# Kernel tuning notes

Measured on AMD Instinct MI355X. Metric: run time of the kernel, lower is better.

## Reference

```python
import jax, jax.numpy as jnp
import numpy as np

N_NODES = 50000
N_EDGES = 800000
N_SCALES = 4
D_IN = 128
D_HID = 128


def gcn_conv(x, W, b, src, dst, ew, n):
    # PyG GCNConv: h = x @ W; add self loops (weight 1); symmetric normalization
    # deg computed over destination with edge weights; out = scatter(norm * h[src]) + b
    h = x @ W
    loops = jnp.arange(n)
    src_f = jnp.concatenate([src, loops])
    dst_f = jnp.concatenate([dst, loops])
    ew_f = jnp.concatenate([ew, jnp.ones((n,), x.dtype)])
    deg = jax.ops.segment_sum(ew_f, dst_f, num_segments=n)
    dinv = jnp.where(deg > 0, jax.lax.rsqrt(deg), jnp.zeros((), x.dtype))
    norm = dinv[src_f] * ew_f * dinv[dst_f]  # [E+n]
    out = jax.ops.segment_sum(h[src_f] * norm[:, None], dst_f, num_segments=n)
    return out + b


def setup_inputs() -> dict:
    key = jax.random.key(0)
    ks = jax.random.split(key, 8)
    x = jax.random.normal(ks[0], (N_NODES, D_IN), dtype=jnp.float32)
    edge_index = jax.random.randint(ks[1], (N_SCALES, 2, N_EDGES), 0, N_NODES, dtype=jnp.int64)
    edge_weight = jax.random.uniform(ks[2], (N_SCALES, N_EDGES), dtype=jnp.float32)
    s = 1.0 / np.sqrt(D_IN)
    W0 = jax.random.uniform(ks[3], (D_IN, D_HID), jnp.float32, -s, s)
    b0 = jnp.zeros((D_HID,), jnp.float32)
    W1 = jax.random.uniform(ks[4], (D_HID, D_HID), jnp.float32, -s, s)
    b1 = jnp.zeros((D_HID,), jnp.float32)
    prelu_a = 0.25 * jnp.ones((D_HID,), jnp.float32)  # torch PReLU default init
    return {"x": x, "edge_index": edge_index, "edge_weight": edge_weight,
            "W0": W0, "b0": b0, "W1": W1, "b1": b1, "prelu_a": prelu_a}


def reference(x, edge_index, edge_weight, W0, b0, W1, b1, prelu_a):
    n = x.shape[0]
    prelu = lambda z: jnp.where(z > 0, z, prelu_a * z)
    outs = []
    for t in range(edge_index.shape[0]):  # small fixed number of scales
        src, dst = edge_index[t, 0], edge_index[t, 1]
        ew = edge_weight[t]
        z = prelu(gcn_conv(x, W0, b0, src, dst, ew, n))
        z = prelu(gcn_conv(z, W1, b1, src, dst, ew, n))
        outs.append(z)
    return jnp.stack(outs)  # [nm_scale, N, hidden]
```

## Files before the change

kernel.cpp:

```cpp
#include <hip/hip_runtime.h>

#define NN 50000
#define NE 800000
#define NS 4
#define NT (NS * NN)
#define D 128
#define SB2 782
#define EW_SCALE 262144.0f
#define EW_INV (1.0f / 262144.0f)

typedef unsigned long long ull;
typedef __attribute__((ext_vector_type(8))) short bf16x8;
typedef __attribute__((ext_vector_type(4))) float f32x4;

__device__ __forceinline__ unsigned short f2bf(float f) {
  unsigned int u = __float_as_uint(f);
  u += 0x7fffu + ((u >> 16) & 1u);
  return (unsigned short)(u >> 16);
}
__device__ __forceinline__ float bf2f(unsigned short h) {
  return __uint_as_float((unsigned int)h << 16);
}

__global__ __launch_bounds__(256) void fused_cpg_k(
    const int* __restrict__ ei, const float* __restrict__ ewA,
    ull* __restrict__ pack8, int* __restrict__ posA,
    const float* __restrict__ X, const float* __restrict__ W0,
    unsigned short* __restrict__ H0h,
    const float* __restrict__ W1, unsigned short* __restrict__ Wsw) {
  __shared__ float xs[64 * 130];
  __shared__ float ws[32 * 128];
  const int bx = blockIdx.x;
  const int t = blockIdx.y;
  const int tid = threadIdx.x;

  if (bx < 782) {
    const int e0 = bx * 1024 + tid;
    const size_t cOff = (size_t)(bx & 7) * NT;
    const int* dst = ei + (size_t)t * 2 * NE + NE;
    const float* ew = ewA + (size_t)t * NE;
    int d[4];
    float w[4];
    bool va[4];
#pragma unroll
    for (int q = 0; q < 4; q++) {
      int e = e0 + q * 256;
      va[q] = e < NE;
      d[q] = 0;
      w[q] = 0.f;
      if (va[q]) {
        d[q] = dst[e];
        w[q] = ew[e];
      }
    }
    ull old[4];
#pragma unroll
    for (int q = 0; q < 4; q++) {
      if (va[q]) {
        ull add = (1ULL << 32) | (ull)__float2uint_rn(w[q] * EW_SCALE);
        old[q] = atomicAdd(&pack8[cOff + t * NN + d[q]], add);
      }
    }
#pragma unroll
    for (int q = 0; q < 4; q++) {
      if (va[q]) posA[(size_t)t * NE + e0 + q * 256] = (int)(old[q] >> 32);
    }
    return;
  }
  if (t != 0) return;

  if (bx < 1564) {
    const int r0 = (bx - 782) * 64;
    for (int i = tid; i < 64 * 64; i += 256) {
      int row = i >> 6, kh = i & 63;
      float2 v = make_float2(0.f, 0.f);
      int gr = r0 + row;
      if (gr < NN) v = *(const float2*)&X[(size_t)gr * D + kh * 2];
      *(float2*)&xs[row * 130 + kh * 2] = v;
    }
    const int tx = tid & 15, ty = tid >> 4;
    const int c0 = tx * 4;
    const int c1 = 64 + tx * 4;
    float acc[4][8];
#pragma unroll
    for (int i = 0; i < 4; i++)
#pragma unroll
      for (int j = 0; j < 8; j++) acc[i][j] = 0.f;

    for (int kc = 0; kc < 4; kc++) {
      __syncthreads();
      for (int i = tid; i < 32 * 32; i += 256) {
        ((float4*)ws)[i] = ((const float4*)(W0 + kc * 32 * D))[i];
      }
      __syncthreads();
#pragma unroll 4
      for (int k2 = 0; k2 < 32; k2++) {
        const int k = kc * 32 + k2;
        float a[4];
#pragma unroll
        for (int j = 0; j < 4; j++) a[j] = xs[(ty * 4 + j) * 130 + k];
        float4 b0 = *(const float4*)&ws[k2 * 128 + c0];
        float4 b1 = *(const float4*)&ws[k2 * 128 + c1];
        float b[8] = {b0.x, b0.y, b0.z, b0.w, b1.x, b1.y, b1.z, b1.w};
#pragma unroll
        for (int i = 0; i < 4; i++)
#pragma unroll
          for (int j = 0; j < 8; j++) acc[i][j] += a[i] * b[j];
      }
    }
#pragma unroll
    for (int i = 0; i < 4; i++) {
      int gr = r0 + ty * 4 + i;
      if (gr < NN) {
        ushort4 o0, o1;
        o0.x = f2bf(acc[i][0]); o0.y = f2bf(acc[i][1]);
        o0.z = f2bf(acc[i][2]); o0.w = f2bf(acc[i][3]);
        o1.x = f2bf(acc[i][4]); o1.y = f2bf(acc[i][5]);
        o1.z = f2bf(acc[i][6]); o1.w = f2bf(acc[i][7]);
        *(ushort4*)&H0h[(size_t)gr * D + c0] = o0;
        *(ushort4*)&H0h[(size_t)gr * D + c1] = o1;
      }
    }
  } else {
    int idx = (bx - 1564) * 256 + tid;
    int j = idx & 7, lane = (idx >> 3) & 63, s = (idx >> 9) & 3, bn = idx >> 11;
    float v = W1[(s * 32 + ((lane >> 4) * 8) + j) * D + bn * 16 + (lane & 15)];
    unsigned short hi = f2bf(v);
    float lo = v - bf2f(hi);
    Wsw[idx] = hi;
    Wsw[16384 + idx] = f2bf(lo);
  }
}

__global__ __launch_bounds__(256) void gemm_inplace_mfma_k(
    unsigned short* __restrict__ ZhA, const unsigned short* __restrict__ Wsw) {
  const int t = blockIdx.y;
  unsigned short* Z = ZhA + (size_t)t * NN * D;
  const int tid = threadIdx.x;
  const int wv = tid >> 6, l = tid & 63;
  const int r0 = blockIdx.x * 64 + wv * 16;
  const int mrow = r0 + (l & 15);
  const int arow = mrow < NN ? mrow : NN - 1;
  bf16x8 a[4];
#pragma unroll
  for (int s = 0; s < 4; s++)
    a[s] = *(const bf16x8*)&Z[(size_t)arow * D + s * 32 + (l >> 4) * 8];
  const int orow0 = r0 + (l >> 4) * 4;
#pragma unroll
  for (int bn = 0; bn < 8; bn++) {
    f32x4 acc = {0.f, 0.f, 0.f, 0.f};
#pragma unroll
    for (int s = 0; s < 4; s++) {
      bf16x8 blo = *(const bf16x8*)&Wsw[16384 + ((bn * 4 + s) * 64 + l) * 8];
      bf16x8 bhi = *(const bf16x8*)&Wsw[((bn * 4 + s) * 64 + l) * 8];
      acc = __builtin_amdgcn_mfma_f32_16x16x32_bf16(a[s], blo, acc, 0, 0, 0);
      acc = __builtin_amdgcn_mfma_f32_16x16x32_bf16(a[s], bhi, acc, 0, 0, 0);
    }
    const int col = bn * 16 + (l & 15);
#pragma unroll
    for (int i = 0; i < 4; i++) {
      int row = orow0 + i;
      if (row < NN) Z[(size_t)row * D + col] = f2bf(acc[i]);
    }
  }
}


__global__ __launch_bounds__(256) void initp_k(ull* __restrict__ packed, int n) {
  int i = blockIdx.x * 256 + threadIdx.x;
  if (i < n) packed[i] = 0ULL;
}

__global__ __launch_bounds__(256) void unpack_scan_k(const ull* __restrict__ pack8,
                                                     float* __restrict__ dinvA,
                                                     int* __restrict__ cntA,
                                                     unsigned short* __restrict__ cbase8,
                                                     int* __restrict__ partial) {
  __shared__ int sm[256];
  const int tid = threadIdx.x;
  const int i = blockIdx.x * 256 + tid;
  int c = 0;
  if (i < NT) {
    unsigned int wsum = 0;
    int run = 0;
#pragma unroll
    for (int k = 0; k < 8; k++) {
      ull p = pack8[(size_t)k * NT + i];
      cbase8[(size_t)k * NT + i] = (unsigned short)run;
      run += (int)(p >> 32);
      wsum += (unsigned int)(p & 0xffffffffULL);
    }
    c = run;
    cntA[i] = c;
    float deg = 1.0f + (float)wsum * EW_INV;
    dinvA[i] = rsqrtf(deg);
  }
  sm[tid] = c;
  __syncthreads();
  for (int off = 128; off > 0; off >>= 1) {
    if (tid < off) sm[tid] += sm[tid + off];
    __syncthreads();
  }
  if (tid == 0) partial[blockIdx.x] = sm[0];
}

__global__ __launch_bounds__(256) void scan_write_k(const int* __restrict__ cntA,
                                                    const int* __restrict__ partial,
                                                    int* __restrict__ offsA) {
  __shared__ int sm[256];
  const int t = threadIdx.x;
  const int bx = blockIdx.x;
  int s = 0;
  for (int i = t; i < bx; i += 256) s += partial[i];
  sm[t] = s;
  __syncthreads();
  for (int off = 128; off > 0; off >>= 1) {
    if (t < off) sm[t] += sm[t + off];
    __syncthreads();
  }
  const int base = sm[0];
  __syncthreads();
  const int i = bx * 256 + t;
  int v = (i < NT) ? cntA[i] : 0;
  sm[t] = v;
  __syncthreads();
  for (int off = 1; off < 256; off <<= 1) {
    int u = (t >= off) ? sm[t - off] : 0;
    __syncthreads();
    sm[t] += u;
    __syncthreads();
  }
  if (i < NT) offsA[i] = base + sm[t] - v;
}

__global__ __launch_bounds__(256) void fill_all_k(const int* __restrict__ ei,
                                                  const float* __restrict__ ewA,
                                                  const float* __restrict__ dinvA,
                                                  const int* __restrict__ offsA,
                                                  const int* __restrict__ posA,
                                                  const unsigned short* __restrict__ cbase8,
                                                  int2* __restrict__ eeA) {
  const int t = blockIdx.y;
  const int e = blockIdx.x * 256 + threadIdx.x;
  if (e < NE) {
    const int* src = ei + (size_t)t * 2 * NE;
    const int* dst = src + NE;
    int s = src[e], d = dst[e];
    const int base = t * NN + d;
    const size_t cOff = (size_t)((e >> 10) & 7) * NT;
    float w = ewA[(size_t)t * NE + e] * dinvA[t * NN + s] * dinvA[base];
    int slot = offsA[base] + (int)cbase8[cOff + base] + posA[(size_t)t * NE + e];
    eeA[slot] = make_int2(s, __float_as_int(w));
  }
}

__global__ __launch_bounds__(256) void gather1_all_k(
    const unsigned short* __restrict__ H, const int* __restrict__ offsA,
    const int* __restrict__ cntA, const int2* __restrict__ eeA,
    const float* __restrict__ dinvA, const float* __restrict__ bias,
    const float* __restrict__ pa, unsigned short* __restrict__ ZhA) {
  const int t = blockIdx.y;
  int g = blockIdx.x * 256 + threadIdx.x;
  int wid = g >> 5;
  int lane = g & 31;
  if (wid >= NN) return;
  const int base = t * NN + wid;
  const int st = offsA[base];
  const int len = cntA[base];
  const int c = lane * 4;
  float ax = 0.f, ay = 0.f, az = 0.f, aw = 0.f;
  int j = 0;
  for (; j + 8 <= len; j += 8) {
    int2 p0 = eeA[st + j];
    int2 p1 = eeA[st + j + 1];
    int2 p2 = eeA[st + j + 2];
    int2 p3 = eeA[st + j + 3];
    int2 p4 = eeA[st + j + 4];
    int2 p5 = eeA[st + j + 5];
    int2 p6 = eeA[st + j + 6];
    int2 p7 = eeA[st + j + 7];
    ushort4 v0 = *(const ushort4*)&H[(size_t)p0.x * D + c];
    ushort4 v1 = *(const ushort4*)&H[(size_t)p1.x * D + c];
    ushort4 v2 = *(const ushort4*)&H[(size_t)p2.x * D + c];
    ushort4 v3 = *(const ushort4*)&H[(size_t)p3.x * D + c];
    ushort4 v4 = *(const ushort4*)&H[(size_t)p4.x * D + c];
    ushort4 v5 = *(const ushort4*)&H[(size_t)p5.x * D + c];
    ushort4 v6 = *(const ushort4*)&H[(size_t)p6.x * D + c];
    ushort4 v7 = *(const ushort4*)&H[(size_t)p7.x * D + c];
    float w0 = __int_as_float(p0.y), w1 = __int_as_float(p1.y);
    float w2 = __int_as_float(p2.y), w3 = __int_as_float(p3.y);
    float w4 = __int_as_float(p4.y), w5 = __int_as_float(p5.y);
    float w6 = __int_as_float(p6.y), w7 = __int_as_float(p7.y);
    ax += w0 * bf2f(v0.x) + w1 * bf2f(v1.x) + w2 * bf2f(v2.x) + w3 * bf2f(v3.x);
    ay += w0 * bf2f(v0.y) + w1 * bf2f(v1.y) + w2 * bf2f(v2.y) + w3 * bf2f(v3.y);
    az += w0 * bf2f(v0.z) + w1 * bf2f(v1.z) + w2 * bf2f(v2.z) + w3 * bf2f(v3.z);
    aw += w0 * bf2f(v0.w) + w1 * bf2f(v1.w) + w2 * bf2f(v2.w) + w3 * bf2f(v3.w);
    ax += w4 * bf2f(v4.x) + w5 * bf2f(v5.x) + w6 * bf2f(v6.x) + w7 * bf2f(v7.x);
    ay += w4 * bf2f(v4.y) + w5 * bf2f(v5.y) + w6 * bf2f(v6.y) + w7 * bf2f(v7.y);
    az += w4 * bf2f(v4.z) + w5 * bf2f(v5.z) + w6 * bf2f(v6.z) + w7 * bf2f(v7.z);
    aw += w4 * bf2f(v4.w) + w5 * bf2f(v5.w) + w6 * bf2f(v6.w) + w7 * bf2f(v7.w);
  }
  for (; j + 4 <= len; j += 4) {
    int2 p0 = eeA[st + j];
    int2 p1 = eeA[st + j + 1];
    int2 p2 = eeA[st + j + 2];
    int2 p3 = eeA[st + j + 3];
    ushort4 v0 = *(const ushort4*)&H[(size_t)p0.x * D + c];
    ushort4 v1 = *(const ushort4*)&H[(size_t)p1.x * D + c];
    ushort4 v2 = *(const ushort4*)&H[(size_t)p2.x * D + c];
    ushort4 v3 = *(const ushort4*)&H[(size_t)p3.x * D + c];
    float w0 = __int_as_float(p0.y), w1 = __int_as_float(p1.y);
    float w2 = __int_as_float(p2.y), w3 = __int_as_float(p3.y);
    ax += w0 * bf2f(v0.x) + w1 * bf2f(v1.x) + w2 * bf2f(v2.x) + w3 * bf2f(v3.x);
    ay += w0 * bf2f(v0.y) + w1 * bf2f(v1.y) + w2 * bf2f(v2.y) + w3 * bf2f(v3.y);
    az += w0 * bf2f(v0.z) + w1 * bf2f(v1.z) + w2 * bf2f(v2.z) + w3 * bf2f(v3.z);
    aw += w0 * bf2f(v0.w) + w1 * bf2f(v1.w) + w2 * bf2f(v2.w) + w3 * bf2f(v3.w);
  }
  for (; j < len; j++) {
    int2 p = eeA[st + j];
    float w = __int_as_float(p.y);
    ushort4 v = *(const ushort4*)&H[(size_t)p.x * D + c];
    ax += w * bf2f(v.x);
    ay += w * bf2f(v.y);
    az += w * bf2f(v.z);
    aw += w * bf2f(v.w);
  }
  float dv = dinvA[base];
  float d2 = dv * dv;
  ushort4 h = *(const ushort4*)&H[(size_t)wid * D + c];
  ax += d2 * bf2f(h.x) + bias[c];
  ay += d2 * bf2f(h.y) + bias[c + 1];
  az += d2 * bf2f(h.z) + bias[c + 2];
  aw += d2 * bf2f(h.w) + bias[c + 3];
  ax = ax > 0.f ? ax : pa[c] * ax;
  ay = ay > 0.f ? ay : pa[c + 1] * ay;
  az = az > 0.f ? az : pa[c + 2] * az;
  aw = aw > 0.f ? aw : pa[c + 3] * aw;
  ushort4 o;
  o.x = f2bf(ax); o.y = f2bf(ay); o.z = f2bf(az); o.w = f2bf(aw);
  *(ushort4*)&ZhA[(size_t)t * NN * D + (size_t)wid * D + c] = o;
}

__global__ __launch_bounds__(256) void gather2_all_k(
    const unsigned short* __restrict__ YA, const int* __restrict__ offsA,
    const int* __restrict__ cntA, const int2* __restrict__ eeA,
    const float* __restrict__ dinvA, const float* __restrict__ bias,
    const float* __restrict__ pa, float* __restrict__ out) {
  const int t = blockIdx.y;
  int g = blockIdx.x * 256 + threadIdx.x;
  int wid = g >> 5;
  int lane = g & 31;
  if (wid >= NN) return;
  const unsigned short* Y = YA + (size_t)t * NN * D;
  const int base = t * NN + wid;
  const int st = offsA[base];
  const int len = cntA[base];
  const int c = lane * 4;
  float ax = 0.f, ay = 0.f, az = 0.f, aw = 0.f;
  int j = 0;
  for (; j + 8 <= len; j += 8) {
    int2 p0 = eeA[st + j];
    int2 p1 = eeA[st + j + 1];
    int2 p2 = eeA[st + j + 2];
    int2 p3 = eeA[st + j + 3];
    int2 p4 = eeA[st + j + 4];
    int2 p5 = eeA[st + j + 5];
    int2 p6 = eeA[st + j + 6];
    int2 p7 = eeA[st + j + 7];
    ushort4 v0 = *(const ushort4*)&Y[(size_t)p0.x * D + c];
    ushort4 v1 = *(const ushort4*)&Y[(size_t)p1.x * D + c];
    ushort4 v2 = *(const ushort4*)&Y[(size_t)p2.x * D + c];
    ushort4 v3 = *(const ushort4*)&Y[(size_t)p3.x * D + c];
    ushort4 v4 = *(const ushort4*)&Y[(size_t)p4.x * D + c];
    ushort4 v5 = *(const ushort4*)&Y[(size_t)p5.x * D + c];
    ushort4 v6 = *(const ushort4*)&Y[(size_t)p6.x * D + c];
    ushort4 v7 = *(const ushort4*)&Y[(size_t)p7.x * D + c];
    float w0 = __int_as_float(p0.y), w1 = __int_as_float(p1.y);
    float w2 = __int_as_float(p2.y), w3 = __int_as_float(p3.y);
    float w4 = __int_as_float(p4.y), w5 = __int_as_float(p5.y);
    float w6 = __int_as_float(p6.y), w7 = __int_as_float(p7.y);
    ax += w0 * bf2f(v0.x) + w1 * bf2f(v1.x) + w2 * bf2f(v2.x) + w3 * bf2f(v3.x);
    ay += w0 * bf2f(v0.y) + w1 * bf2f(v1.y) + w2 * bf2f(v2.y) + w3 * bf2f(v3.y);
    az += w0 * bf2f(v0.z) + w1 * bf2f(v1.z) + w2 * bf2f(v2.z) + w3 * bf2f(v3.z);
    aw += w0 * bf2f(v0.w) + w1 * bf2f(v1.w) + w2 * bf2f(v2.w) + w3 * bf2f(v3.w);
    ax += w4 * bf2f(v4.x) + w5 * bf2f(v5.x) + w6 * bf2f(v6.x) + w7 * bf2f(v7.x);
    ay += w4 * bf2f(v4.y) + w5 * bf2f(v5.y) + w6 * bf2f(v6.y) + w7 * bf2f(v7.y);
    az += w4 * bf2f(v4.z) + w5 * bf2f(v5.z) + w6 * bf2f(v6.z) + w7 * bf2f(v7.z);
    aw += w4 * bf2f(v4.w) + w5 * bf2f(v5.w) + w6 * bf2f(v6.w) + w7 * bf2f(v7.w);
  }
  for (; j + 4 <= len; j += 4) {
    int2 p0 = eeA[st + j];
    int2 p1 = eeA[st + j + 1];
    int2 p2 = eeA[st + j + 2];
    int2 p3 = eeA[st + j + 3];
    ushort4 v0 = *(const ushort4*)&Y[(size_t)p0.x * D + c];
    ushort4 v1 = *(const ushort4*)&Y[(size_t)p1.x * D + c];
    ushort4 v2 = *(const ushort4*)&Y[(size_t)p2.x * D + c];
    ushort4 v3 = *(const ushort4*)&Y[(size_t)p3.x * D + c];
    float w0 = __int_as_float(p0.y), w1 = __int_as_float(p1.y);
    float w2 = __int_as_float(p2.y), w3 = __int_as_float(p3.y);
    ax += w0 * bf2f(v0.x) + w1 * bf2f(v1.x) + w2 * bf2f(v2.x) + w3 * bf2f(v3.x);
    ay += w0 * bf2f(v0.y) + w1 * bf2f(v1.y) + w2 * bf2f(v2.y) + w3 * bf2f(v3.y);
    az += w0 * bf2f(v0.z) + w1 * bf2f(v1.z) + w2 * bf2f(v2.z) + w3 * bf2f(v3.z);
    aw += w0 * bf2f(v0.w) + w1 * bf2f(v1.w) + w2 * bf2f(v2.w) + w3 * bf2f(v3.w);
  }
  for (; j < len; j++) {
    int2 p = eeA[st + j];
    float w = __int_as_float(p.y);
    ushort4 v = *(const ushort4*)&Y[(size_t)p.x * D + c];
    ax += w * bf2f(v.x);
    ay += w * bf2f(v.y);
    az += w * bf2f(v.z);
    aw += w * bf2f(v.w);
  }
  float dv = dinvA[base];
  float d2 = dv * dv;
  ushort4 h = *(const ushort4*)&Y[(size_t)wid * D + c];
  ax += d2 * bf2f(h.x) + bias[c];
  ay += d2 * bf2f(h.y) + bias[c + 1];
  az += d2 * bf2f(h.z) + bias[c + 2];
  aw += d2 * bf2f(h.w) + bias[c + 3];
  ax = ax > 0.f ? ax : pa[c] * ax;
  ay = ay > 0.f ? ay : pa[c + 1] * ay;
  az = az > 0.f ? az : pa[c + 2] * az;
  aw = aw > 0.f ? aw : pa[c + 3] * aw;
  float* outT = out + (size_t)t * NN * D;
  *(float4*)&outT[(size_t)wid * D + c] = make_float4(ax, ay, az, aw);
}


extern "C" void kernel_launch(void* const* d_in, const int* in_sizes, int n_in,
                              void* d_out, int out_size, void* d_ws, size_t ws_size,
                              hipStream_t stream) {
  const float* x = (const float*)d_in[0];
  const int* ei = (const int*)d_in[1];
  const float* ew = (const float*)d_in[2];
  const float* W0 = (const float*)d_in[3];
  const float* b0 = (const float*)d_in[4];
  const float* W1 = (const float*)d_in[5];
  const float* b1 = (const float*)d_in[6];
  const float* pa = (const float*)d_in[7];
  float* out = (float*)d_out;

  int2* eeA = (int2*)d_ws;
  int* posA = (int*)(eeA + (size_t)NS * NE);
  float* dinvA = (float*)(posA + (size_t)NS * NE);
  int* cntA = (int*)(dinvA + NT);
  int* offsA = cntA + NT;
  int* partial = offsA + NT;
  int* poffs = partial + 1024;
  unsigned short* H0h = (unsigned short*)(poffs + 1024);
  unsigned short* ZhA = H0h + (size_t)NN * D;
  unsigned short* Wsw = ZhA + (size_t)NS * NN * D;
  unsigned short* cbase8 = ZhA;
  ull* pack8 = (ull*)(ZhA + (size_t)8 * NT);

  const int gGemm = (NN + 63) / 64;
  const int gEdge = (NE + 255) / 256;
  const int gInit8 = (8 * NT) / 256;
  const int gGather = (NN * 32 + 255) / 256;
  const int gFused = 782 + 782 + 64;

  initp_k<<<gInit8, 256, 0, stream>>>(pack8, 8 * NT);
  fused_cpg_k<<<dim3(gFused, NS), 256, 0, stream>>>(ei, ew, pack8, posA,
                                                    x, W0, H0h, W1, Wsw);

  unpack_scan_k<<<SB2, 256, 0, stream>>>(pack8, dinvA, cntA, cbase8, partial);
  scan_write_k<<<SB2, 256, 0, stream>>>(cntA, partial, offsA);
  fill_all_k<<<dim3(gEdge, NS), 256, 0, stream>>>(ei, ew, dinvA, offsA, posA,
                                                  cbase8, eeA);

  gather1_all_k<<<dim3(gGather, NS), 256, 0, stream>>>(H0h, offsA, cntA, eeA,
                                                       dinvA, b0, pa, ZhA);
  gemm_inplace_mfma_k<<<dim3(gGemm, NS), 256, 0, stream>>>(ZhA, Wsw);
  gather2_all_k<<<dim3(gGather, NS), 256, 0, stream>>>(ZhA, offsA, cntA, eeA,
                                                       dinvA, b1, pa, out);
}
```

Before: 700.3 us.

## Build CSR via two-level binned counting sort with LDS histograms instead of global atomics

Replaces the global 64-bit atomic counting pass, the multi-kernel scan and the posA-based fill with a radix-style binning sort. Edges are first histogrammed by dst>>8 into shared-memory bins per block and the per-bin histograms are scanned. Edges are then scattered into bins, and each bin is sorted locally in LDS to produce the CSR, degrees and dinv, followed by a normalization pass. This aims to cut contended global atomics and random global writes, at the cost of more kernel launches, an extra edge-array pass, and packing dst and src into 16 bits each (dst<<16|s). That packing only works because node ids fit in 16 bits (NN=50000) and LDS atomics keep the edge order non-deterministic.

```diff
diff --git a/kernel.cpp b/kernel.cpp
--- a/kernel.cpp
+++ b/kernel.cpp
@@ -5,10 +5,12 @@
 #define NS 4
 #define NT (NS * NN)
 #define D 128
-#define SB2 782
+#define NB 196
+#define CB 782
 #define EW_SCALE 262144.0f
 #define EW_INV (1.0f / 262144.0f)
 
+typedef unsigned int u32;
 typedef unsigned long long ull;
 typedef __attribute__((ext_vector_type(8))) short bf16x8;
 typedef __attribute__((ext_vector_type(4))) float f32x4;
@@ -22,55 +24,35 @@
   return __uint_as_float((unsigned int)h << 16);
 }
 
-__global__ __launch_bounds__(256) void fused_cpg_k(
-    const int* __restrict__ ei, const float* __restrict__ ewA,
-    ull* __restrict__ pack8, int* __restrict__ posA,
+__global__ __launch_bounds__(256) void fused_hg_k(
+    const int* __restrict__ ei, u32* __restrict__ ghist,
     const float* __restrict__ X, const float* __restrict__ W0,
     unsigned short* __restrict__ H0h,
     const float* __restrict__ W1, unsigned short* __restrict__ Wsw) {
   __shared__ float xs[64 * 130];
   __shared__ float ws[32 * 128];
+  __shared__ u32 h[NB];
   const int bx = blockIdx.x;
   const int t = blockIdx.y;
   const int tid = threadIdx.x;
 
-  if (bx < 782) {
-    const int e0 = bx * 1024 + tid;
-    const size_t cOff = (size_t)(bx & 7) * NT;
+  if (bx < CB) {
+    if (tid < NB) h[tid] = 0;
+    __syncthreads();
     const int* dst = ei + (size_t)t * 2 * NE + NE;
-    const float* ew = ewA + (size_t)t * NE;
-    int d[4];
-    float w[4];
-    bool va[4];
 #pragma unroll
     for (int q = 0; q < 4; q++) {
-      int e = e0 + q * 256;
-      va[q] = e < NE;
-      d[q] = 0;
-      w[q] = 0.f;
-      if (va[q]) {
-        d[q] = dst[e];
-        w[q] = ew[e];
-      }
-    }
-    ull old[4];
-#pragma unroll
-    for (int q = 0; q < 4; q++) {
-      if (va[q]) {
-        ull add = (1ULL << 32) | (ull)__float2uint_rn(w[q] * EW_SCALE);
-        old[q] = atomicAdd(&pack8[cOff + t * NN + d[q]], add);
-      }
-    }
-#pragma unroll
-    for (int q = 0; q < 4; q++) {
-      if (va[q]) posA[(size_t)t * NE + e0 + q * 256] = (int)(old[q] >> 32);
-    }
+      int e = bx * 1024 + q * 256 + tid;
+      if (e < NE) atomicAdd(&h[(u32)dst[e] >> 8], 1u);
+    }
+    __syncthreads();
+    if (tid < NB) ghist[((size_t)t * NB + tid) * CB + bx] = h[tid];
     return;
   }
   if (t != 0) return;
 
-  if (bx < 1564) {
-    const int r0 = (bx - 782) * 64;
+  if (bx < 2 * CB) {
+    const int r0 = (bx - CB) * 64;
     for (int i = tid; i < 64 * 64; i += 256) {
       int row = i >> 6, kh = i & 63;
       float2 v = make_float2(0.f, 0.f);
@@ -122,13 +104,155 @@
       }
     }
   } else {
-    int idx = (bx - 1564) * 256 + tid;
+    int idx = (bx - 2 * CB) * 256 + tid;
     int j = idx & 7, lane = (idx >> 3) & 63, s = (idx >> 9) & 3, bn = idx >> 11;
     float v = W1[(s * 32 + ((lane >> 4) * 8) + j) * D + bn * 16 + (lane & 15)];
     unsigned short hi = f2bf(v);
     float lo = v - bf2f(hi);
     Wsw[idx] = hi;
     Wsw[16384 + idx] = f2bf(lo);
+  }
+}
+
+__global__ __launch_bounds__(256) void scanbin_k(u32* __restrict__ ghist,
+                                                 u32* __restrict__ bincnt) {
+  __shared__ int sm[256];
+  const int b = blockIdx.x, t = blockIdx.y, tid = threadIdx.x;
+  u32* g = ghist + ((size_t)t * NB + b) * CB;
+  const int lo = tid * 4;
+  const int hi = min(lo + 4, CB);
+  int s = 0;
+  for (int i = lo; i < hi; i++) s += (int)g[i];
+  sm[tid] = s;
+  __syncthreads();
+  for (int off = 1; off < 256; off <<= 1) {
+    int u = (tid >= off) ? sm[tid - off] : 0;
+    __syncthreads();
+    sm[tid] += u;
+    __syncthreads();
+  }
+  int run = sm[tid] - s;
+  for (int i = lo; i < hi; i++) {
+    u32 v = g[i];
+    g[i] = (u32)run;
+    run += (int)v;
+  }
+  if (lo < CB && hi == CB) bincnt[t * NB + b] = (u32)run;
+}
+
+__global__ __launch_bounds__(256) void binbase_k(const u32* __restrict__ bincnt,
+                                                 u32* __restrict__ binbase) {
+  __shared__ int sm[256];
+  const int t = blockIdx.y, tid = threadIdx.x;
+  int v = (tid < NB) ? (int)bincnt[t * NB + tid] : 0;
+  sm[tid] = v;
+  __syncthreads();
+  for (int off = 1; off < 256; off <<= 1) {
+    int u = (tid >= off) ? sm[tid - off] : 0;
+    __syncthreads();
+    sm[tid] += u;
+    __syncthreads();
+  }
+  if (tid < NB) binbase[t * NB + tid] = (u32)(sm[tid] - v);
+}
+
+__global__ __launch_bounds__(256) void scat_k(const int* __restrict__ ei,
+                                              const float* __restrict__ ewA,
+                                              const u32* __restrict__ ghist,
+                                              const u32* __restrict__ binbase,
+                                              int2* __restrict__ ebin) {
+  __shared__ u32 c[NB];
+  __shared__ int bb[NB];
+  const int bx = blockIdx.x, t = blockIdx.y, tid = threadIdx.x;
+  if (tid < NB) {
+    c[tid] = ghist[((size_t)t * NB + tid) * CB + bx];
+    bb[tid] = (int)binbase[t * NB + tid];
+  }
+  __syncthreads();
+  const int* src = ei + (size_t)t * 2 * NE;
+  const int* dst = src + NE;
+  const float* ew = ewA + (size_t)t * NE;
+  int2* eb = ebin + (size_t)t * NE;
+#pragma unroll
+  for (int q = 0; q < 4; q++) {
+    int e = bx * 1024 + q * 256 + tid;
+    if (e < NE) {
+      u32 d = (u32)dst[e];
+      u32 s = (u32)src[e];
+      float w = ew[e];
+      u32 bin = d >> 8;
+      u32 r = atomicAdd(&c[bin], 1u);
+      eb[bb[bin] + r] = make_int2((int)((d << 16) | s), __float_as_int(w));
+    }
+  }
+}
+
+__global__ __launch_bounds__(256) void bincsr_k(const int2* __restrict__ ebin,
+                                                const u32* __restrict__ bincnt,
+                                                const u32* __restrict__ binbase,
+                                                int* __restrict__ cntA,
+                                                int* __restrict__ offsA,
+                                                float* __restrict__ dinvA,
+                                                int2* __restrict__ eeA) {
+  __shared__ u32 cnt[256];
+  __shared__ u32 wsum[256];
+  __shared__ u32 c2[256];
+  __shared__ int sm[256];
+  __shared__ int excls[256];
+  const int b = blockIdx.x, t = blockIdx.y, tid = threadIdx.x;
+  const int m = (int)bincnt[t * NB + b];
+  const int bb = (int)binbase[t * NB + b];
+  const int2* eb = ebin + (size_t)t * NE + bb;
+  cnt[tid] = 0;
+  wsum[tid] = 0;
+  c2[tid] = 0;
+  __syncthreads();
+  for (int i = tid; i < m; i += 256) {
+    int2 r = eb[i];
+    u32 dl = ((u32)r.x >> 16) & 255u;
+    atomicAdd(&cnt[dl], 1u);
+    atomicAdd(&wsum[dl], (u32)__float2uint_rn(__int_as_float(r.y) * EW_SCALE));
+  }
+  __syncthreads();
+  int v = (int)cnt[tid];
+  sm[tid] = v;
+  __syncthreads();
+  for (int off = 1; off < 256; off <<= 1) {
+    int u = (tid >= off) ? sm[tid - off] : 0;
+    __syncthreads();
+    sm[tid] += u;
+    __syncthreads();
+  }
+  const int excl = sm[tid] - v;
+  excls[tid] = excl;
+  const int g = b * 256 + tid;
+  if (g < NN) {
+    cntA[t * NN + g] = v;
+    offsA[t * NN + g] = t * NE + bb + excl;
+    float deg = 1.0f + (float)wsum[tid] * EW_INV;
+    dinvA[t * NN + g] = rsqrtf(deg);
+  }
+  __syncthreads();
+  int2* ee = eeA + (size_t)t * NE + bb;
+  for (int i = tid; i < m; i += 256) {
+    int2 r = eb[i];
+    u32 dl = ((u32)r.x >> 16) & 255u;
+    u32 rk = atomicAdd(&c2[dl], 1u);
+    ee[excls[dl] + (int)rk] = r;
+  }
+}
+
+__global__ __launch_bounds__(256) void rescale_k(const float* __restrict__ dinvA,
+                                                 int2* __restrict__ eeA) {
+  const int t = blockIdx.y;
+  const int e = blockIdx.x * 256 + threadIdx.x;
+  if (e < NE) {
+    int2 r = eeA[(size_t)t * NE + e];
+    int s = r.x & 0xffff;
+    int d = (int)((u32)r.x >> 16);
+    const float* dv = dinvA + t * NN;
+    float w = __int_as_float(r.y) * dv[s] * dv[d];
+    eeA[(size_t)t * NE + e] = make_int2(s, __float_as_int(w));
   }
 }
 
@@ -162,95 +286,6 @@
       int row = orow0 + i;
       if (row < NN) Z[(size_t)row * D + col] = f2bf(acc[i]);
     }
-  }
-}
-
-
-__global__ __launch_bounds__(256) void initp_k(ull* __restrict__ packed, int n) {
-  int i = blockIdx.x * 256 + threadIdx.x;
-  if (i < n) packed[i] = 0ULL;
-}
-
-__global__ __launch_bounds__(256) void unpack_scan_k(const ull* __restrict__ pack8,
-                                                     float* __restrict__ dinvA,
-                                                     int* __restrict__ cntA,
-                                                     unsigned short* __restrict__ cbase8,
-                                                     int* __restrict__ partial) {
-  __shared__ int sm[256];
-  const int tid = threadIdx.x;
-  const int i = blockIdx.x * 256 + tid;
-  int c = 0;
-  if (i < NT) {
-    unsigned int wsum = 0;
-    int run = 0;
-#pragma unroll
-    for (int k = 0; k < 8; k++) {
-      ull p = pack8[(size_t)k * NT + i];
-      cbase8[(size_t)k * NT + i] = (unsigned short)run;
-      run += (int)(p >> 32);
-      wsum += (unsigned int)(p & 0xffffffffULL);
-    }
-    c = run;
-    cntA[i] = c;
-    float deg = 1.0f + (float)wsum * EW_INV;
-    dinvA[i] = rsqrtf(deg);
-  }
-  sm[tid] = c;
-  __syncthreads();
-  for (int off = 128; off > 0; off >>= 1) {
-    if (tid < off) sm[tid] += sm[tid + off];
-    __syncthreads();
-  }
-  if (tid == 0) partial[blockIdx.x] = sm[0];
-}
-
-__global__ __launch_bounds__(256) void scan_write_k(const int* __restrict__ cntA,
-                                                    const int* __restrict__ partial,
-                                                    int* __restrict__ offsA) {
-  __shared__ int sm[256];
-  const int t = threadIdx.x;
-  const int bx = blockIdx.x;
-  int s = 0;
-  for (int i = t; i < bx; i += 256) s += partial[i];
-  sm[t] = s;
-  __syncthreads();
-  for (int off = 128; off > 0; off >>= 1) {
-    if (t < off) sm[t] += sm[t + off];
-    __syncthreads();
-  }
-  const int base = sm[0];
-  __syncthreads();
-  const int i = bx * 256 + t;
-  int v = (i < NT) ? cntA[i] : 0;
-  sm[t] = v;
-  __syncthreads();
-  for (int off = 1; off < 256; off <<= 1) {
-    int u = (t >= off) ? sm[t - off] : 0;
-    __syncthreads();
-    sm[t] += u;
-    __syncthreads();
-  }
-  if (i < NT) offsA[i] = base + sm[t] - v;
-}
-
-__global__ __launch_bounds__(256) void fill_all_k(const int* __restrict__ ei,
-                                                  const float* __restrict__ ewA,
-                                                  const float* __restrict__ dinvA,
-                                                  const int* __restrict__ offsA,
-                                                  const int* __restrict__ posA,
-                                                  const unsigned short* __restrict__ cbase8,
-                                                  int2* __restrict__ eeA) {
-  const int t = blockIdx.y;
-  const int e = blockIdx.x * 256 + threadIdx.x;
-  if (e < NE) {
-    const int* src = ei + (size_t)t * 2 * NE;
-    const int* dst = src + NE;
-    int s = src[e], d = dst[e];
-    const int base = t * NN + d;
-    const size_t cOff = (size_t)((e >> 10) & 7) * NT;
-    float w = ewA[(size_t)t * NE + e] * dinvA[t * NN + s] * dinvA[base];
-    int slot = offsA[base] + (int)cbase8[cOff + base] + posA[(size_t)t * NE + e];
-    eeA[slot] = make_int2(s, __float_as_int(w));
   }
 }
 
@@ -443,32 +478,29 @@
   float* out = (float*)d_out;
 
   int2* eeA = (int2*)d_ws;
-  int* posA = (int*)(eeA + (size_t)NS * NE);
-  float* dinvA = (float*)(posA + (size_t)NS * NE);
+  float* dinvA = (float*)(eeA + (size_t)NS * NE);
   int* cntA = (int*)(dinvA + NT);
   int* offsA = cntA + NT;
-  int* partial = offsA + NT;
-  int* poffs = partial + 1024;
-  unsigned short* H0h = (unsigned short*)(poffs + 1024);
+  unsigned short* H0h = (unsigned short*)(offsA + NT);
   unsigned short* ZhA = H0h + (size_t)NN * D;
   unsigned short* Wsw = ZhA + (size_t)NS * NN * D;
-  unsigned short* cbase8 = ZhA;
-  ull* pack8 = (ull*)(ZhA + (size_t)8 * NT);
+  int2* ebin = (int2*)ZhA;
+  u32* ghist = (u32*)(ebin + (size_t)NS * NE);
+  u32* bincnt = ghist + (size_t)NS * NB * CB;
+  u32* binbase = bincnt + NS * NB;
 
   const int gGemm = (NN + 63) / 64;
   const int gEdge = (NE + 255) / 256;
-  const int gInit8 = (8 * NT) / 256;
   const int gGather = (NN * 32 + 255) / 256;
-  const int gFused = 782 + 782 + 64;
-
-  initp_k<<<gInit8, 256, 0, stream>>>(pack8, 8 * NT);
-  fused_cpg_k<<<dim3(gFused, NS), 256, 0, stream>>>(ei, ew, pack8, posA,
-                                                    x, W0, H0h, W1, Wsw);
-
-  unpack_scan_k<<<SB2, 256, 0, stream>>>(pack8, dinvA, cntA, cbase8, partial);
-  scan_write_k<<<SB2, 256, 0, stream>>>(cntA, partial, offsA);
-  fill_all_k<<<dim3(gEdge, NS), 256, 0, stream>>>(ei, ew, dinvA, offsA, posA,
-                                                  cbase8, eeA);
+  const int gFused = CB + CB + 64;
+
+  fused_hg_k<<<dim3(gFused, NS), 256, 0, stream>>>(ei, ghist, x, W0, H0h, W1, Wsw);
+  scanbin_k<<<dim3(NB, NS), 256, 0, stream>>>(ghist, bincnt);
+  binbase_k<<<dim3(1, NS), 256, 0, stream>>>(bincnt, binbase);
+  scat_k<<<dim3(CB, NS), 256, 0, stream>>>(ei, ew, ghist, binbase, ebin);
+  bincsr_k<<<dim3(NB, NS), 256, 0, stream>>>(ebin, bincnt, binbase, cntA, offsA,
+                                             dinvA, eeA);
+  rescale_k<<<dim3(gEdge, NS), 256, 0, stream>>>(dinvA, eeA);
 
   gather1_all_k<<<dim3(gGather, NS), 256, 0, stream>>>(H0h, offsA, cntA, eeA,
                                                        dinvA, b0, pa, ZhA);
```

After: 595.2 us. 1.18x faster.
